# Kernel tuning notes

Hardware: AMD Instinct MI355X
Metric: run time of the kernel (lower is better)

## Reference

```python
import jax, jax.numpy as jnp
import numpy as np

N_NODES = 30000
N_EDGES = 480000
N_GRAPHS = 64
NEG_SLOPE = 0.2
BN_EPS = 1e-5


def _leaky_relu(x, slope=NEG_SLOPE):
    return jnp.where(x >= 0, x, slope * x)


def gat_layer(x, src, dst, W, att_src, att_dst, bias, heads, ch, n_nodes):
    # x: [N, F_in]; W: [F_in, heads*ch]
    h = (x @ W).reshape(n_nodes, heads, ch)            # [N,H,C]
    a_s = jnp.sum(h * att_src, axis=-1)                # [N,H]
    a_d = jnp.sum(h * att_dst, axis=-1)                # [N,H]
    e = _leaky_relu(a_s[src] + a_d[dst])               # [E,H] per-edge logits
    # edge-softmax over incoming edges of each destination node
    m = jax.ops.segment_max(e, dst, num_segments=n_nodes)   # [N,H]
    ex = jnp.exp(e - m[dst])
    denom = jax.ops.segment_sum(ex, dst, num_segments=n_nodes)
    alpha = ex / denom[dst]                            # [E,H]
    msg = alpha[:, :, None] * h[src]                   # [E,H,C]
    out = jax.ops.segment_sum(msg, dst, num_segments=n_nodes)  # [N,H,C]
    return out.reshape(n_nodes, heads * ch) + bias


def setup_inputs() -> dict:
    key = jax.random.key(0)
    ks = jax.random.split(key, 16)
    x = jax.random.normal(ks[0], (N_NODES, 3), dtype=jnp.float32)
    edge_index = jax.random.randint(ks[1], (2, N_EDGES), 0, N_NODES, dtype=jnp.int64)
    batch = jnp.sort(jax.random.randint(ks[2], (N_NODES,), 0, N_GRAPHS, dtype=jnp.int64))

    def glorot(k, shape):
        fan = shape[0] + shape[-1]
        s = jnp.sqrt(6.0 / fan)
        return jax.random.uniform(k, shape, jnp.float32, -s, s)

    params = dict(
        W1=glorot(ks[3], (3, 8 * 64)),
        att_src1=glorot(ks[4], (8, 64)) * 0.1,
        att_dst1=glorot(ks[5], (8, 64)) * 0.1,
        b1=jnp.zeros((8 * 64,), jnp.float32),
        W2=glorot(ks[6], (8 * 64, 4 * 32)),
        att_src2=glorot(ks[7], (4, 32)) * 0.1,
        att_dst2=glorot(ks[8], (4, 32)) * 0.1,
        b2=jnp.zeros((4 * 32,), jnp.float32),
        Wfc=glorot(ks[9], (4 * 32, 32)),
        bfc=jnp.zeros((32,), jnp.float32),
        bn_gamma=jnp.ones((32,), jnp.float32),
        bn_beta=jnp.zeros((32,), jnp.float32),
        Wheat=glorot(ks[10], (32, 3)),
        bheat=jnp.zeros((3,), jnp.float32),
        Wdehyd=glorot(ks[11], (32, 2)),
        bdehyd=jnp.zeros((2,), jnp.float32),
    )
    return {"x": x, "edge_index": edge_index, "batch": batch, **params}


def reference(x, edge_index, batch, W1, att_src1, att_dst1, b1,
              W2, att_src2, att_dst2, b2, Wfc, bfc, bn_gamma, bn_beta,
              Wheat, bheat, Wdehyd, bdehyd):
    n = x.shape[0]
    # GATConv adds self-loops by default
    loops = jnp.arange(n, dtype=edge_index.dtype)
    src = jnp.concatenate([edge_index[0], loops])
    dst = jnp.concatenate([edge_index[1], loops])

    x1 = jax.nn.relu(gat_layer(x, src, dst, W1, att_src1, att_dst1, b1, 8, 64, n))   # [N,512]
    x2 = jax.nn.relu(gat_layer(x1, src, dst, W2, att_src2, att_dst2, b2, 4, 32, n))  # [N,128]
    h = x1[:, : x2.shape[1]] + x2                                                    # [N,128]

    # global_mean_pool over graph ids
    sums = jax.ops.segment_sum(h, batch, num_segments=N_GRAPHS)                      # [G,128]
    cnts = jax.ops.segment_sum(jnp.ones((n,), h.dtype), batch, num_segments=N_GRAPHS)
    pooled = sums / jnp.maximum(cnts, 1.0)[:, None]

    z = pooled @ Wfc + bfc                                                           # [G,32]
    mu = jnp.mean(z, axis=0)
    var = jnp.var(z, axis=0)
    z = bn_gamma * (z - mu) / jnp.sqrt(var + BN_EPS) + bn_beta
    z = jax.nn.relu(z)
    return (z @ Wheat + bheat, z @ Wdehyd + bdehyd)
```

## Files before the change

### kernel.cpp

```cpp
#include <hip/hip_runtime.h>
#include <math.h>


#define N_NODES 30000
#define N_GRAPHS 64

__global__ __launch_bounds__(256) void k_att1(
    const float* __restrict__ x, const float* __restrict__ W1,
    const float* __restrict__ asw, const float* __restrict__ adw,
    float* __restrict__ a_s, float* __restrict__ a_d, int n)
{
    __shared__ float Ps[24], Pd[24];
    int t = threadIdx.x;
    if (t < 48) {
        int which = t / 24;
        int idx = t - which * 24;
        int d = idx >> 3, h = idx & 7;
        const float* av = (which ? adw : asw) + h * 64;
        const float* wr = W1 + d * 512 + h * 64;
        float s = 0.f;
        #pragma unroll 8
        for (int c = 0; c < 64; ++c) s = fmaf(wr[c], av[c], s);
        (which ? Pd : Ps)[idx] = s;
    }
    __syncthreads();
    int node = blockIdx.x * 256 + t;
    if (node >= n) return;
    float x0 = x[node * 3 + 0];
    float x1v = x[node * 3 + 1];
    float x2v = x[node * 3 + 2];
    #pragma unroll
    for (int h = 0; h < 8; ++h) {
        a_s[node * 8 + h] = fmaf(x0, Ps[h], fmaf(x1v, Ps[8 + h], x2v * Ps[16 + h]));
        a_d[node * 8 + h] = fmaf(x0, Pd[h], fmaf(x1v, Pd[8 + h], x2v * Pd[16 + h]));
    }
}

__global__ void k_deg(const int* __restrict__ ei, int* __restrict__ deg,
                      int E0, int n)
{
    int e = blockIdx.x * blockDim.x + threadIdx.x;
    int Et = E0 + n;
    if (e >= Et) return;
    int dst = (e < E0) ? ei[E0 + e] : (e - E0);
    atomicAdd(&deg[dst], 1);
}

__global__ __launch_bounds__(1024) void k_scan(
    const int* __restrict__ deg, int* __restrict__ rowstart,
    int* __restrict__ cursor, int n)
{
    __shared__ int wsum[16];
    __shared__ int woff[17];
    __shared__ int carry_s;
    int tid = threadIdx.x, lane = tid & 63, wid = tid >> 6;
    if (tid == 0) carry_s = 0;
    __syncthreads();
    int nchunks = (n + 1023) >> 10;
    for (int c = 0; c < nchunks; ++c) {
        int i = (c << 10) + tid;
        int v = (i < n) ? deg[i] : 0;
        int s = v;
        #pragma unroll
        for (int off = 1; off < 64; off <<= 1) {
            int t = __shfl_up(s, off);
            if (lane >= off) s += t;
        }
        if (lane == 63) wsum[wid] = s;
        __syncthreads();
        if (wid == 0) {
            int ws = (lane < 16) ? wsum[lane] : 0;
            #pragma unroll
            for (int off = 1; off < 16; off <<= 1) {
                int t = __shfl_up(ws, off);
                if (lane >= off) ws += t;
            }
            if (lane < 16) woff[lane + 1] = ws;
            if (lane == 0) woff[0] = 0;
        }
        __syncthreads();
        int excl = carry_s + woff[wid] + s - v;
        if (i < n) { rowstart[i] = excl; cursor[i] = excl; }
        __syncthreads();
        if (tid == 0) carry_s += woff[16];
        __syncthreads();
    }
    if (tid == 0) rowstart[n] = carry_s;
}

__global__ void k_fill(const int* __restrict__ ei, int* __restrict__ cursor,
                       int* __restrict__ csr, int E0, int n)
{
    int e = blockIdx.x * blockDim.x + threadIdx.x;
    int Et = E0 + n;
    if (e >= Et) return;
    int src, dst;
    if (e < E0) { src = ei[e]; dst = ei[E0 + e]; }
    else        { src = e - E0; dst = e - E0; }
    int pos = atomicAdd(&cursor[dst], 1);
    csr[pos] = src;
}

__global__ __launch_bounds__(256) void k_gat1(
    const float* __restrict__ x, const float* __restrict__ a_s,
    const float* __restrict__ a_d, const int* __restrict__ rowstart,
    const int* __restrict__ csr, float* __restrict__ Shat, int n)
{
    int lane = threadIdx.x & 63;
    int node = blockIdx.x * 4 + (threadIdx.x >> 6);
    if (node >= n) return;
    int rs = rowstart[node], re = rowstart[node + 1];
    int hd = lane >> 3;
    int slot = lane & 7;
    float adn = a_d[node * 8 + hd];

    float m = -1e30f, ssum = 0.f, S0 = 0.f, S1 = 0.f, S2 = 0.f;
    for (int i = rs + slot; i < re; i += 8) {
        int src = csr[i];
        float e = a_s[src * 8 + hd] + adn;
        e = (e >= 0.f) ? e : 0.2f * e;
        float x0 = x[src * 3 + 0];
        float x1v = x[src * 3 + 1];
        float x2v = x[src * 3 + 2];
        float mn = fmaxf(m, e);
        float sc = __expf(m - mn);
        float wgt = __expf(e - mn);
        ssum = fmaf(ssum, sc, wgt);
        S0 = fmaf(S0, sc, wgt * x0);
        S1 = fmaf(S1, sc, wgt * x1v);
        S2 = fmaf(S2, sc, wgt * x2v);
        m = mn;
    }
    #pragma unroll
    for (int off = 1; off < 8; off <<= 1) {
        float mo = __shfl_xor(m, off);
        float so = __shfl_xor(ssum, off);
        float t0 = __shfl_xor(S0, off);
        float t1 = __shfl_xor(S1, off);
        float t2 = __shfl_xor(S2, off);
        float mn = fmaxf(m, mo);
        float scA = __expf(m - mn);
        float scB = __expf(mo - mn);
        ssum = ssum * scA + so * scB;
        S0 = S0 * scA + t0 * scB;
        S1 = S1 * scA + t1 * scB;
        S2 = S2 * scA + t2 * scB;
        m = mn;
    }
    if (slot == 0) {
        float inv = 1.f / ssum;
        float4 o;
        o.x = S0 * inv; o.y = S1 * inv; o.z = S2 * inv; o.w = 0.f;
        *(float4*)(Shat + ((size_t)node * 8 + hd) * 4) = o;
    }
}

#define GM_BM 32
#define GM_BK 32
#define GM_APAD 36
__global__ __launch_bounds__(256) void k_gemm2(
    const float* __restrict__ Shat, const float* __restrict__ W1,
    const float* __restrict__ bias1, const float* __restrict__ W2,
    const float* __restrict__ asw, const float* __restrict__ adw,
    float* __restrict__ h2, float* __restrict__ a_s2, float* __restrict__ a_d2,
    int n)
{
    __shared__ float As[GM_BK][GM_APAD];
    __shared__ float Bs[GM_BK][128];
    int tid = threadIdx.x;
    int tr = tid >> 5;
    int tc = tid & 31;
    int bm = blockIdx.x * GM_BM;

    int sRow = tid & 31;
    int sK4  = (tid >> 5) << 2;
    int srowg = bm + sRow; if (srowg >= n) srowg = n - 1;
    const float* shp = Shat + (size_t)srowg * 32;

    float acc[4][4];
    #pragma unroll
    for (int r = 0; r < 4; ++r)
        #pragma unroll
        for (int c = 0; c < 4; ++c) acc[r][c] = 0.f;

    for (int s = 0; s < 16; ++s) {
        int k0 = s * GM_BK;
        {
            int kg = k0 + sK4;
            float4 sh = *(const float4*)(shp + ((kg >> 6) << 2));
            float4 w0 = *(const float4*)(W1 + kg);
            float4 w1v = *(const float4*)(W1 + 512 + kg);
            float4 w2v = *(const float4*)(W1 + 1024 + kg);
            float4 bb = *(const float4*)(bias1 + kg);
            As[sK4 + 0][sRow] = fmaxf(fmaf(sh.x, w0.x, fmaf(sh.y, w1v.x, fmaf(sh.z, w2v.x, bb.x))), 0.f);
            As[sK4 + 1][sRow] = fmaxf(fmaf(sh.x, w0.y, fmaf(sh.y, w1v.y, fmaf(sh.z, w2v.y, bb.y))), 0.f);
            As[sK4 + 2][sRow] = fmaxf(fmaf(sh.x, w0.z, fmaf(sh.y, w1v.z, fmaf(sh.z, w2v.z, bb.z))), 0.f);
            As[sK4 + 3][sRow] = fmaxf(fmaf(sh.x, w0.w, fmaf(sh.y, w1v.w, fmaf(sh.z, w2v.w, bb.w))), 0.f);
        }
        #pragma unroll
        for (int j = 0; j < 4; ++j) {
            int li = tid + j * 256;
            *(float4*)(&Bs[li >> 5][(li & 31) * 4]) =
                *(const float4*)(W2 + (size_t)(k0 + (li >> 5)) * 128 + (li & 31) * 4);
        }
        __syncthreads();
        #pragma unroll
        for (int kk = 0; kk < GM_BK; ++kk) {
            float4 a4 = *(const float4*)(&As[kk][tr * 4]);
            float4 b4 = *(const float4*)(&Bs[kk][tc * 4]);
            acc[0][0] = fmaf(a4.x, b4.x, acc[0][0]);
            acc[0][1] = fmaf(a4.x, b4.y, acc[0][1]);
            acc[0][2] = fmaf(a4.x, b4.z, acc[0][2]);
            acc[0][3] = fmaf(a4.x, b4.w, acc[0][3]);
            acc[1][0] = fmaf(a4.y, b4.x, acc[1][0]);
            acc[1][1] = fmaf(a4.y, b4.y, acc[1][1]);
            acc[1][2] = fmaf(a4.y, b4.z, acc[1][2]);
            acc[1][3] = fmaf(a4.y, b4.w, acc[1][3]);
            acc[2][0] = fmaf(a4.z, b4.x, acc[2][0]);
            acc[2][1] = fmaf(a4.z, b4.y, acc[2][1]);
            acc[2][2] = fmaf(a4.z, b4.z, acc[2][2]);
            acc[2][3] = fmaf(a4.z, b4.w, acc[2][3]);
            acc[3][0] = fmaf(a4.w, b4.x, acc[3][0]);
            acc[3][1] = fmaf(a4.w, b4.y, acc[3][1]);
            acc[3][2] = fmaf(a4.w, b4.z, acc[3][2]);
            acc[3][3] = fmaf(a4.w, b4.w, acc[3][3]);
        }
        if (s < 15) __syncthreads();
    }

    #pragma unroll
    for (int r = 0; r < 4; ++r) {
        int row = bm + tr * 4 + r;
        if (row < n) {
            float4 o;
            o.x = acc[r][0]; o.y = acc[r][1]; o.z = acc[r][2]; o.w = acc[r][3];
            *(float4*)(h2 + (size_t)row * 128 + tc * 4) = o;
        }
    }

    float4 ws = *(const float4*)(asw + tc * 4);
    float4 wd = *(const float4*)(adw + tc * 4);
    #pragma unroll
    for (int r = 0; r < 4; ++r) {
        float ps = acc[r][0] * ws.x + acc[r][1] * ws.y + acc[r][2] * ws.z + acc[r][3] * ws.w;
        float pd = acc[r][0] * wd.x + acc[r][1] * wd.y + acc[r][2] * wd.z + acc[r][3] * wd.w;
        ps += __shfl_xor(ps, 1); ps += __shfl_xor(ps, 2); ps += __shfl_xor(ps, 4);
        pd += __shfl_xor(pd, 1); pd += __shfl_xor(pd, 2); pd += __shfl_xor(pd, 4);
        if ((tc & 7) == 0) {
            int row = bm + tr * 4 + r;
            if (row < n) {
                int hd = tc >> 3;
                a_s2[row * 4 + hd] = ps;
                a_d2[row * 4 + hd] = pd;
            }
        }
    }
}

__global__ __launch_bounds__(256) void k_gat2(
    const float* __restrict__ h2, const float* __restrict__ a_s,
    const float* __restrict__ a_d, const int* __restrict__ rowstart,
    const int* __restrict__ csr, const float* __restrict__ bias,
    const float* __restrict__ Shat, const float* __restrict__ W1,
    const float* __restrict__ bias1, float* __restrict__ hres, int n)
{
    int lane = threadIdx.x & 63;
    int node = blockIdx.x * 4 + (threadIdx.x >> 6);
    if (node >= n) return;
    int rs = rowstart[node], re = rowstart[node + 1];
    int hd = lane >> 4;
    float adn = a_d[node * 4 + hd];

    float m = -1e30f, ssum = 0.f, acc0 = 0.f, acc1 = 0.f;
    int src_next = (rs < re) ? csr[rs] : 0;
    for (int i = rs; i < re; ++i) {
        int src = src_next;
        if (i + 1 < re) src_next = csr[i + 1];
        float e = a_s[src * 4 + hd] + adn;
        e = (e >= 0.f) ? e : 0.2f * e;
        float2 hv = *(const float2*)(h2 + (size_t)src * 128 + lane * 2);
        float mn = fmaxf(m, e);
        float sc = __expf(m - mn);
        float wgt = __expf(e - mn);
        ssum = fmaf(ssum, sc, wgt);
        acc0 = fmaf(acc0, sc, wgt * hv.x);
        acc1 = fmaf(acc1, sc, wgt * hv.y);
        m = mn;
    }
    float inv = 1.f / ssum;

    int hh = lane >> 5;
    float4 shv = *(const float4*)(Shat + ((size_t)node * 8 + hh) * 4);
    float2 w0 = *(const float2*)(W1 + lane * 2);
    float2 w1v = *(const float2*)(W1 + 512 + lane * 2);
    float2 w2v = *(const float2*)(W1 + 1024 + lane * 2);
    float2 bv = *(const float2*)(bias1 + lane * 2);
    float r0 = fmaxf(fmaf(shv.x, w0.x, fmaf(shv.y, w1v.x, fmaf(shv.z, w2v.x, bv.x))), 0.f);
    float r1 = fmaxf(fmaf(shv.x, w0.y, fmaf(shv.y, w1v.y, fmaf(shv.z, w2v.y, bv.y))), 0.f);

    float2 o;
    o.x = r0 + fmaxf(fmaf(acc0, inv, bias[lane * 2 + 0]), 0.f);
    o.y = r1 + fmaxf(fmaf(acc1, inv, bias[lane * 2 + 1]), 0.f);
    *(float2*)(hres + (size_t)node * 128 + lane * 2) = o;
}

__global__ __launch_bounds__(128) void k_pool(
    const float* __restrict__ hres, const int* __restrict__ batch,
    float* __restrict__ pooled, float* __restrict__ cnt, int n)
{
    int j = threadIdx.x;
    int n0 = blockIdx.x * 128;
    if (n0 >= n) return;
    int n1 = min(n0 + 128, n);
    int g = batch[n0];
    float acc = 0.f;
    int run = 0;
    for (int node = n0; node < n1; ++node) {
        int gb = batch[node];
        if (gb != g) {
            atomicAdd(&pooled[g * 128 + j], acc);
            if (j == 0) atomicAdd(&cnt[g], (float)run);
            acc = 0.f; run = 0; g = gb;
        }
        acc += hres[(size_t)node * 128 + j];
        run++;
    }
    atomicAdd(&pooled[g * 128 + j], acc);
    if (j == 0) atomicAdd(&cnt[g], (float)run);
}

__global__ __launch_bounds__(1024) void k_head(
    const float* __restrict__ pooled, const float* __restrict__ cnt,
    const float* __restrict__ Wfc, const float* __restrict__ bfc,
    const float* __restrict__ gamma, const float* __restrict__ beta,
    const float* __restrict__ Wheat, const float* __restrict__ bheat,
    const float* __restrict__ Wdehyd, const float* __restrict__ bdehyd,
    float* __restrict__ out)
{
    __shared__ float z[N_GRAPHS * 32];
    __shared__ float mu_s[32], rstd_s[32];
    int t = threadIdx.x;
    for (int idx = t; idx < N_GRAPHS * 32; idx += 1024) {
        int g = idx >> 5, j = idx & 31;
        float c = cnt[g];
        c = c < 1.f ? 1.f : c;
        float s = 0.f;
        for (int k = 0; k < 128; ++k)
            s = fmaf(pooled[g * 128 + k], Wfc[k * 32 + j], s);
        z[idx] = s / c + bfc[j];
    }
    __syncthreads();
    if (t < 32) {
        float mu = 0.f;
        for (int g = 0; g < N_GRAPHS; ++g) mu += z[g * 32 + t];
        mu *= (1.f / N_GRAPHS);
        float var = 0.f;
        for (int g = 0; g < N_GRAPHS; ++g) {
            float d = z[g * 32 + t] - mu;
            var = fmaf(d, d, var);
        }
        var *= (1.f / N_GRAPHS);
        mu_s[t] = mu;
        rstd_s[t] = 1.f / sqrtf(var + 1e-5f);
    }
    __syncthreads();
    for (int idx = t; idx < N_GRAPHS * 32; idx += 1024) {
        int j = idx & 31;
        float v = gamma[j] * (z[idx] - mu_s[j]) * rstd_s[j] + beta[j];
        z[idx] = v > 0.f ? v : 0.f;
    }
    __syncthreads();
    if (t < N_GRAPHS * 3) {
        int g = t / 3, r = t - g * 3;
        float s = 0.f;
        for (int j2 = 0; j2 < 32; ++j2)
            s = fmaf(z[g * 32 + j2], Wheat[j2 * 3 + r], s);
        out[t] = s + bheat[r];
    } else if (t < N_GRAPHS * 3 + N_GRAPHS * 2) {
        int idx = t - N_GRAPHS * 3;
        int g = idx >> 1, r = idx & 1;
        float s = 0.f;
        for (int j2 = 0; j2 < 32; ++j2)
            s = fmaf(z[g * 32 + j2], Wdehyd[j2 * 2 + r], s);
        out[N_GRAPHS * 3 + idx] = s + bdehyd[r];
    }
}

extern "C" void kernel_launch(void* const* d_in, const int* in_sizes, int n_in,
                              void* d_out, int out_size, void* d_ws, size_t ws_size,
                              hipStream_t stream)
{
    const float* x      = (const float*)d_in[0];
    const int*   ei     = (const int*)d_in[1];
    const int*   batch  = (const int*)d_in[2];
    const float* W1     = (const float*)d_in[3];
    const float* as1w   = (const float*)d_in[4];
    const float* ad1w   = (const float*)d_in[5];
    const float* b1     = (const float*)d_in[6];
    const float* W2     = (const float*)d_in[7];
    const float* as2w   = (const float*)d_in[8];
    const float* ad2w   = (const float*)d_in[9];
    const float* b2     = (const float*)d_in[10];
    const float* Wfc    = (const float*)d_in[11];
    const float* bfc    = (const float*)d_in[12];
    const float* gamma  = (const float*)d_in[13];
    const float* beta   = (const float*)d_in[14];
    const float* Wheat  = (const float*)d_in[15];
    const float* bheat  = (const float*)d_in[16];
    const float* Wdehyd = (const float*)d_in[17];
    const float* bdehyd = (const float*)d_in[18];
    float* out = (float*)d_out;

    const int N = N_NODES;
    const int E0 = in_sizes[1] / 2;
    const int Et = E0 + N;
    const int G = N_GRAPHS;

    char* w = (char*)d_ws;
    auto alloc = [&](size_t bytes) -> char* {
        char* p = w;
        w += (bytes + 255) & ~(size_t)255;
        return p;
    };
    float* Shat  = (float*)alloc((size_t)N * 32 * 4);
    float* h2    = (float*)alloc((size_t)N * 128 * 4);
    float* hres  = (float*)alloc((size_t)N * 128 * 4);
    float* a_s1  = (float*)alloc((size_t)N * 8 * 4);
    float* a_d1  = (float*)alloc((size_t)N * 8 * 4);
    float* a_s2  = (float*)alloc((size_t)N * 4 * 4);
    float* a_d2  = (float*)alloc((size_t)N * 4 * 4);
    int* deg     = (int*)alloc((size_t)(N + 1) * 4);
    int* rowstart= (int*)alloc((size_t)(N + 1) * 4);
    int* cursor  = (int*)alloc((size_t)N * 4);
    int* csr     = (int*)alloc((size_t)Et * 4);
    float* pooled= (float*)alloc((size_t)G * 128 * 4);
    float* cntf  = (float*)alloc((size_t)G * 4);

    hipMemsetAsync(deg, 0, (size_t)(N + 1) * 4, stream);
    hipMemsetAsync(pooled, 0, (size_t)G * 128 * 4, stream);
    hipMemsetAsync(cntf, 0, (size_t)G * 4, stream);

    k_att1<<<(N + 255) / 256, 256, 0, stream>>>(x, W1, as1w, ad1w, a_s1, a_d1, N);
    k_deg<<<(Et + 255) / 256, 256, 0, stream>>>(ei, deg, E0, N);
    k_scan<<<1, 1024, 0, stream>>>(deg, rowstart, cursor, N);
    k_fill<<<(Et + 255) / 256, 256, 0, stream>>>(ei, cursor, csr, E0, N);
    k_gat1<<<(N + 3) / 4, 256, 0, stream>>>(x, a_s1, a_d1, rowstart, csr, Shat, N);
    k_gemm2<<<(N + GM_BM - 1) / GM_BM, 256, 0, stream>>>(Shat, W1, b1, W2, as2w, ad2w, h2, a_s2, a_d2, N);
    k_gat2<<<(N + 3) / 4, 256, 0, stream>>>(h2, a_s2, a_d2, rowstart, csr, b2, Shat, W1, b1, hres, N);
    k_pool<<<(N + 127) / 128, 128, 0, stream>>>(hres, batch, pooled, cntf, N);
    k_head<<<1, 1024, 0, stream>>>(pooled, cntf, Wfc, bfc, gamma, beta,
                                   Wheat, bheat, Wdehyd, bdehyd, out);
}
```

Measured before the change: 415.4 us.

## Split-K GEMM with 8x8 register tiles and drop online-softmax max tracking

The layer-2 GEMM becomes a split-K kernel with 128-row tiles, 8x8 per-thread register blocking and four K slices. Each slice writes partial results to a new workspace buffer, and a separate reduction kernel sums the slices and computes the attention dot products. Both GAT aggregation loops now accumulate plain exp(e) sums instead of running an online softmax with max rescaling, which removes extra exps and the max-merge shuffles. The costs are roughly 61MB of extra partial-result traffic, one more launch, and possible overflow in exp for large logits, although small attention weights make that unlikely here.

```diff
diff --git a/kernel.cpp b/kernel.cpp
--- a/kernel.cpp
+++ b/kernel.cpp
@@ -63,8 +63,8 @@
         int s = v;
         #pragma unroll
         for (int off = 1; off < 64; off <<= 1) {
-            int t = __shfl_up(s, off);
-            if (lane >= off) s += t;
+            int t2 = __shfl_up(s, off);
+            if (lane >= off) s += t2;
         }
         if (lane == 63) wsum[wid] = s;
         __syncthreads();
@@ -72,8 +72,8 @@
             int ws = (lane < 16) ? wsum[lane] : 0;
             #pragma unroll
             for (int off = 1; off < 16; off <<= 1) {
-                int t = __shfl_up(ws, off);
-                if (lane >= off) ws += t;
+                int t2 = __shfl_up(ws, off);
+                if (lane >= off) ws += t2;
             }
             if (lane < 16) woff[lane + 1] = ws;
             if (lane == 0) woff[0] = 0;
@@ -114,38 +114,23 @@
     int slot = lane & 7;
     float adn = a_d[node * 8 + hd];
 
-    float m = -1e30f, ssum = 0.f, S0 = 0.f, S1 = 0.f, S2 = 0.f;
+    float ssum = 0.f, S0 = 0.f, S1 = 0.f, S2 = 0.f;
     for (int i = rs + slot; i < re; i += 8) {
         int src = csr[i];
         float e = a_s[src * 8 + hd] + adn;
         e = (e >= 0.f) ? e : 0.2f * e;
-        float x0 = x[src * 3 + 0];
-        float x1v = x[src * 3 + 1];
-        float x2v = x[src * 3 + 2];
-        float mn = fmaxf(m, e);
-        float sc = __expf(m - mn);
-        float wgt = __expf(e - mn);
-        ssum = fmaf(ssum, sc, wgt);
-        S0 = fmaf(S0, sc, wgt * x0);
-        S1 = fmaf(S1, sc, wgt * x1v);
-        S2 = fmaf(S2, sc, wgt * x2v);
-        m = mn;
+        float w = __expf(e);
+        ssum += w;
+        S0 = fmaf(w, x[src * 3 + 0], S0);
+        S1 = fmaf(w, x[src * 3 + 1], S1);
+        S2 = fmaf(w, x[src * 3 + 2], S2);
     }
     #pragma unroll
     for (int off = 1; off < 8; off <<= 1) {
-        float mo = __shfl_xor(m, off);
-        float so = __shfl_xor(ssum, off);
-        float t0 = __shfl_xor(S0, off);
-        float t1 = __shfl_xor(S1, off);
-        float t2 = __shfl_xor(S2, off);
-        float mn = fmaxf(m, mo);
-        float scA = __expf(m - mn);
-        float scB = __expf(mo - mn);
-        ssum = ssum * scA + so * scB;
-        S0 = S0 * scA + t0 * scB;
-        S1 = S1 * scA + t1 * scB;
-        S2 = S2 * scA + t2 * scB;
-        m = mn;
+        ssum += __shfl_xor(ssum, off);
+        S0 += __shfl_xor(S0, off);
+        S1 += __shfl_xor(S1, off);
+        S2 += __shfl_xor(S2, off);
     }
     if (slot == 0) {
         float inv = 1.f / ssum;
@@ -155,47 +140,52 @@
     }
 }
 
-#define GM_BM 32
-#define GM_BK 32
-#define GM_APAD 36
-__global__ __launch_bounds__(256) void k_gemm2(
+#define KS_NK 4
+#define KS_BM 128
+#define KS_BK 32
+#define KS_APAD 132
+__global__ __launch_bounds__(256) void k_gemm2ks(
     const float* __restrict__ Shat, const float* __restrict__ W1,
     const float* __restrict__ bias1, const float* __restrict__ W2,
-    const float* __restrict__ asw, const float* __restrict__ adw,
-    float* __restrict__ h2, float* __restrict__ a_s2, float* __restrict__ a_d2,
-    int n)
-{
-    __shared__ float As[GM_BK][GM_APAD];
-    __shared__ float Bs[GM_BK][128];
+    float* __restrict__ P, int n)
+{
+    __shared__ float As[KS_BK][KS_APAD];
+    __shared__ float Bs[KS_BK][128];
     int tid = threadIdx.x;
-    int tr = tid >> 5;
-    int tc = tid & 31;
-    int bm = blockIdx.x * GM_BM;
-
-    int sRow = tid & 31;
-    int sK4  = (tid >> 5) << 2;
+    int bs = blockIdx.x;
+    int ks = bs & 3;
+    int bm = (bs >> 2) * KS_BM;
+
+    int tr = tid >> 4;
+    int tc = tid & 15;
+    int sRow = tid & 127;
+    int sKg = (tid >> 7) << 4;
     int srowg = bm + sRow; if (srowg >= n) srowg = n - 1;
     const float* shp = Shat + (size_t)srowg * 32;
 
-    float acc[4][4];
+    float acc[8][8];
     #pragma unroll
-    for (int r = 0; r < 4; ++r)
+    for (int r = 0; r < 8; ++r)
         #pragma unroll
-        for (int c = 0; c < 4; ++c) acc[r][c] = 0.f;
-
-    for (int s = 0; s < 16; ++s) {
-        int k0 = s * GM_BK;
+        for (int c = 0; c < 8; ++c) acc[r][c] = 0.f;
+
+    for (int s = 0; s < 4; ++s) {
+        int k0 = ks * 128 + s * KS_BK;
+        int head = k0 >> 6;
         {
-            int kg = k0 + sK4;
-            float4 sh = *(const float4*)(shp + ((kg >> 6) << 2));
-            float4 w0 = *(const float4*)(W1 + kg);
-            float4 w1v = *(const float4*)(W1 + 512 + kg);
-            float4 w2v = *(const float4*)(W1 + 1024 + kg);
-            float4 bb = *(const float4*)(bias1 + kg);
-            As[sK4 + 0][sRow] = fmaxf(fmaf(sh.x, w0.x, fmaf(sh.y, w1v.x, fmaf(sh.z, w2v.x, bb.x))), 0.f);
-            As[sK4 + 1][sRow] = fmaxf(fmaf(sh.x, w0.y, fmaf(sh.y, w1v.y, fmaf(sh.z, w2v.y, bb.y))), 0.f);
-            As[sK4 + 2][sRow] = fmaxf(fmaf(sh.x, w0.z, fmaf(sh.y, w1v.z, fmaf(sh.z, w2v.z, bb.z))), 0.f);
-            As[sK4 + 3][sRow] = fmaxf(fmaf(sh.x, w0.w, fmaf(sh.y, w1v.w, fmaf(sh.z, w2v.w, bb.w))), 0.f);
+            float4 sh = *(const float4*)(shp + head * 4);
+            int kb = k0 + sKg;
+            #pragma unroll
+            for (int q = 0; q < 4; ++q) {
+                float4 w0 = *(const float4*)(W1 + kb + q * 4);
+                float4 w1v = *(const float4*)(W1 + 512 + kb + q * 4);
+                float4 w2v = *(const float4*)(W1 + 1024 + kb + q * 4);
+                float4 bb = *(const float4*)(bias1 + kb + q * 4);
+                As[sKg + q * 4 + 0][sRow] = fmaxf(fmaf(sh.x, w0.x, fmaf(sh.y, w1v.x, fmaf(sh.z, w2v.x, bb.x))), 0.f);
+                As[sKg + q * 4 + 1][sRow] = fmaxf(fmaf(sh.x, w0.y, fmaf(sh.y, w1v.y, fmaf(sh.z, w2v.y, bb.y))), 0.f);
+                As[sKg + q * 4 + 2][sRow] = fmaxf(fmaf(sh.x, w0.z, fmaf(sh.y, w1v.z, fmaf(sh.z, w2v.z, bb.z))), 0.f);
+                As[sKg + q * 4 + 3][sRow] = fmaxf(fmaf(sh.x, w0.w, fmaf(sh.y, w1v.w, fmaf(sh.z, w2v.w, bb.w))), 0.f);
+            }
         }
         #pragma unroll
         for (int j = 0; j < 4; ++j) {
@@ -205,55 +195,68 @@
         }
         __syncthreads();
         #pragma unroll
-        for (int kk = 0; kk < GM_BK; ++kk) {
-            float4 a4 = *(const float4*)(&As[kk][tr * 4]);
-            float4 b4 = *(const float4*)(&Bs[kk][tc * 4]);
-            acc[0][0] = fmaf(a4.x, b4.x, acc[0][0]);
-            acc[0][1] = fmaf(a4.x, b4.y, acc[0][1]);
-            acc[0][2] = fmaf(a4.x, b4.z, acc[0][2]);
-            acc[0][3] = fmaf(a4.x, b4.w, acc[0][3]);
-            acc[1][0] = fmaf(a4.y, b4.x, acc[1][0]);
-            acc[1][1] = fmaf(a4.y, b4.y, acc[1][1]);
-            acc[1][2] = fmaf(a4.y, b4.z, acc[1][2]);
-            acc[1][3] = fmaf(a4.y, b4.w, acc[1][3]);
-            acc[2][0] = fmaf(a4.z, b4.x, acc[2][0]);
-            acc[2][1] = fmaf(a4.z, b4.y, acc[2][1]);
-            acc[2][2] = fmaf(a4.z, b4.z, acc[2][2]);
-            acc[2][3] = fmaf(a4.z, b4.w, acc[2][3]);
-            acc[3][0] = fmaf(a4.w, b4.x, acc[3][0]);
-            acc[3][1] = fmaf(a4.w, b4.y, acc[3][1]);
-            acc[3][2] = fmaf(a4.w, b4.z, acc[3][2]);
-            acc[3][3] = fmaf(a4.w, b4.w, acc[3][3]);
-        }
-        if (s < 15) __syncthreads();
-    }
-
+        for (int kk = 0; kk < KS_BK; ++kk) {
+            float4 aL = *(const float4*)(&As[kk][tr * 8]);
+            float4 aH = *(const float4*)(&As[kk][tr * 8 + 4]);
+            float4 bL = *(const float4*)(&Bs[kk][tc * 4]);
+            float4 bH = *(const float4*)(&Bs[kk][64 + tc * 4]);
+            float av[8] = {aL.x, aL.y, aL.z, aL.w, aH.x, aH.y, aH.z, aH.w};
+            float bv[8] = {bL.x, bL.y, bL.z, bL.w, bH.x, bH.y, bH.z, bH.w};
+            #pragma unroll
+            for (int r = 0; r < 8; ++r)
+                #pragma unroll
+                for (int c = 0; c < 8; ++c)
+                    acc[r][c] = fmaf(av[r], bv[c], acc[r][c]);
+        }
+        if (s < 3) __syncthreads();
+    }
+
+    float* Pk = P + (size_t)ks * n * 128;
     #pragma unroll
-    for (int r = 0; r < 4; ++r) {
-        int row = bm + tr * 4 + r;
+    for (int r = 0; r < 8; ++r) {
+        int row = bm + tr * 8 + r;
         if (row < n) {
-            float4 o;
-            o.x = acc[r][0]; o.y = acc[r][1]; o.z = acc[r][2]; o.w = acc[r][3];
-            *(float4*)(h2 + (size_t)row * 128 + tc * 4) = o;
-        }
-    }
+            float4 oL, oH;
+            oL.x = acc[r][0]; oL.y = acc[r][1]; oL.z = acc[r][2]; oL.w = acc[r][3];
+            oH.x = acc[r][4]; oH.y = acc[r][5]; oH.z = acc[r][6]; oH.w = acc[r][7];
+            *(float4*)(Pk + (size_t)row * 128 + tc * 4) = oL;
+            *(float4*)(Pk + (size_t)row * 128 + 64 + tc * 4) = oH;
+        }
+    }
+}
+
+__global__ __launch_bounds__(256) void k_gred(
+    const float* __restrict__ P, const float* __restrict__ asw,
+    const float* __restrict__ adw, float* __restrict__ h2,
+    float* __restrict__ a_s2, float* __restrict__ a_d2, int n)
+{
+    int gi = blockIdx.x * 256 + threadIdx.x;
+    int row = gi >> 5;
+    int tc = gi & 31;
+    if (row >= n) return;
+    size_t off = (size_t)row * 128 + tc * 4;
+    size_t stride = (size_t)n * 128;
+    float4 p0 = *(const float4*)(P + off);
+    float4 p1 = *(const float4*)(P + stride + off);
+    float4 p2 = *(const float4*)(P + 2 * stride + off);
+    float4 p3 = *(const float4*)(P + 3 * stride + off);
+    float4 o;
+    o.x = (p0.x + p1.x) + (p2.x + p3.x);
+    o.y = (p0.y + p1.y) + (p2.y + p3.y);
+    o.z = (p0.z + p1.z) + (p2.z + p3.z);
+    o.w = (p0.w + p1.w) + (p2.w + p3.w);
+    *(float4*)(h2 + off) = o;
 
     float4 ws = *(const float4*)(asw + tc * 4);
     float4 wd = *(const float4*)(adw + tc * 4);
-    #pragma unroll
-    for (int r = 0; r < 4; ++r) {
-        float ps = acc[r][0] * ws.x + acc[r][1] * ws.y + acc[r][2] * ws.z + acc[r][3] * ws.w;
-        float pd = acc[r][0] * wd.x + acc[r][1] * wd.y + acc[r][2] * wd.z + acc[r][3] * wd.w;
-        ps += __shfl_xor(ps, 1); ps += __shfl_xor(ps, 2); ps += __shfl_xor(ps, 4);
-        pd += __shfl_xor(pd, 1); pd += __shfl_xor(pd, 2); pd += __shfl_xor(pd, 4);
-        if ((tc & 7) == 0) {
-            int row = bm + tr * 4 + r;
-            if (row < n) {
-                int hd = tc >> 3;
-                a_s2[row * 4 + hd] = ps;
-                a_d2[row * 4 + hd] = pd;
-            }
-        }
+    float ps = o.x * ws.x + o.y * ws.y + o.z * ws.z + o.w * ws.w;
+    float pd = o.x * wd.x + o.y * wd.y + o.z * wd.z + o.w * wd.w;
+    ps += __shfl_xor(ps, 1); ps += __shfl_xor(ps, 2); ps += __shfl_xor(ps, 4);
+    pd += __shfl_xor(pd, 1); pd += __shfl_xor(pd, 2); pd += __shfl_xor(pd, 4);
+    if ((tc & 7) == 0) {
+        int hd = tc >> 3;
+        a_s2[row * 4 + hd] = ps;
+        a_d2[row * 4 + hd] = pd;
     }
 }
 
@@ -271,21 +274,18 @@
     int hd = lane >> 4;
     float adn = a_d[node * 4 + hd];
 
-    float m = -1e30f, ssum = 0.f, acc0 = 0.f, acc1 = 0.f;
+    float ssum = 0.f, acc0 = 0.f, acc1 = 0.f;
     int src_next = (rs < re) ? csr[rs] : 0;
     for (int i = rs; i < re; ++i) {
         int src = src_next;
         if (i + 1 < re) src_next = csr[i + 1];
         float e = a_s[src * 4 + hd] + adn;
         e = (e >= 0.f) ? e : 0.2f * e;
+        float w = __expf(e);
         float2 hv = *(const float2*)(h2 + (size_t)src * 128 + lane * 2);
-        float mn = fmaxf(m, e);
-        float sc = __expf(m - mn);
-        float wgt = __expf(e - mn);
-        ssum = fmaf(ssum, sc, wgt);
-        acc0 = fmaf(acc0, sc, wgt * hv.x);
-        acc1 = fmaf(acc1, sc, wgt * hv.y);
-        m = mn;
+        ssum += w;
+        acc0 = fmaf(w, hv.x, acc0);
+        acc1 = fmaf(w, hv.y, acc1);
     }
     float inv = 1.f / ssum;
 
@@ -423,6 +423,7 @@
         return p;
     };
     float* Shat  = (float*)alloc((size_t)N * 32 * 4);
+    float* P     = (float*)alloc((size_t)KS_NK * N * 128 * 4);
     float* h2    = (float*)alloc((size_t)N * 128 * 4);
     float* hres  = (float*)alloc((size_t)N * 128 * 4);
     float* a_s1  = (float*)alloc((size_t)N * 8 * 4);
@@ -445,7 +446,9 @@
     k_scan<<<1, 1024, 0, stream>>>(deg, rowstart, cursor, N);
     k_fill<<<(Et + 255) / 256, 256, 0, stream>>>(ei, cursor, csr, E0, N);
     k_gat1<<<(N + 3) / 4, 256, 0, stream>>>(x, a_s1, a_d1, rowstart, csr, Shat, N);
-    k_gemm2<<<(N + GM_BM - 1) / GM_BM, 256, 0, stream>>>(Shat, W1, b1, W2, as2w, ad2w, h2, a_s2, a_d2, N);
+    int rowblocks = (N + KS_BM - 1) / KS_BM;
+    k_gemm2ks<<<rowblocks * KS_NK, 256, 0, stream>>>(Shat, W1, b1, W2, P, N);
+    k_gred<<<(N * 32 + 255) / 256, 256, 0, stream>>>(P, as2w, ad2w, h2, a_s2, a_d2, N);
     k_gat2<<<(N + 3) / 4, 256, 0, stream>>>(h2, a_s2, a_d2, rowstart, csr, b2, Shat, W1, b1, hres, N);
     k_pool<<<(N + 127) / 128, 128, 0, stream>>>(hres, batch, pooled, cntf, N);
     k_head<<<1, 1024, 0, stream>>>(pooled, cntf, Wfc, bfc, gamma, beta,
```

Result: slower. 524.8 us (+26.4%).
